# Performance work log

Measured on AMD Instinct MI355X. Metric: run time of the kernel, lower is better.

## Reference

```python
import jax, jax.numpy as jnp
import numpy as np

B, T, F, H = 64, 2048, 256, 256


def setup_inputs() -> dict:
    key = jax.random.key(0)
    k1, k2, k3 = jax.random.split(key, 3)
    return {
        "carry": jnp.zeros((B, H), jnp.float32),
        "x": jax.random.normal(k1, (B, T, F), jnp.float32),
        "Wi": jax.random.normal(k2, (F, 3 * H), jnp.float32) * (1.0 / np.sqrt(F)),
        "Wh": jax.random.normal(k3, (H, 3 * H), jnp.float32) * (1.0 / np.sqrt(H)),
        "bh": jnp.zeros((3 * H,), jnp.float32),
    }


def reference(carry, x, Wi, Wh, bh):
    # time_major=False: transpose to [T, B, F] for the scan
    xt = jnp.transpose(x, (1, 0, 2))
    # Precompute all input projections in one big GEMM (same math as per-step
    # dense_i since inputs don't depend on the carry): [T, B, 3H]
    xi = jnp.einsum("tbf,fg->tbg", xt, Wi)

    def step(h, xi_t):
        hp = h @ Wh + bh  # recurrent projections (bias on hidden side, as in flax GRUCell)
        i_r, i_z, i_n = jnp.split(xi_t, 3, axis=-1)
        h_r, h_z, h_n = jnp.split(hp, 3, axis=-1)
        r = jax.nn.sigmoid(i_r + h_r)
        z = jax.nn.sigmoid(i_z + h_z)
        n = jnp.tanh(i_n + r * h_n)
        new_h = (1.0 - z) * n + z * h
        return new_h, new_h

    carry, hidden = jax.lax.scan(step, carry, xi, unroll=1)
    hidden = jnp.transpose(hidden, (1, 0, 2))  # back to [B, T, H]
    return carry, hidden
```

## Files before the change

kernel.cpp:

```cpp
#include <hip/hip_runtime.h>
#include <hip/hip_fp16.h>
#include <stdint.h>

#define NB   64
#define NT   2048
#define NF   256
#define NH   256
#define NG   768
#define NPROD 192
#define GRPT  16

typedef unsigned int u32;
typedef _Float16 f16;
typedef f16 half2v __attribute__((ext_vector_type(2)));

__device__ __forceinline__ u32 packpair(float a, float b) {
    return __builtin_bit_cast(u32, __builtin_amdgcn_cvt_pkrtz(a, b));
}
__device__ __forceinline__ float fdot2u(u32 w, u32 h, float acc) {
#if __has_builtin(__builtin_amdgcn_fdot2)
    return __builtin_amdgcn_fdot2(__builtin_bit_cast(half2v, w),
                                  __builtin_bit_cast(half2v, h), acc, false);
#else
    half2v wv = __builtin_bit_cast(half2v, w), hv = __builtin_bit_cast(half2v, h);
    return fmaf((float)wv[1], (float)hv[1], fmaf((float)wv[0], (float)hv[0], acc));
#endif
}
__device__ __forceinline__ u32 hfma2u(u32 w, u32 h, u32 acc) {
    __half2 r = __hfma2(__builtin_bit_cast(__half2, w),
                        __builtin_bit_cast(__half2, h),
                        __builtin_bit_cast(__half2, acc));
    return __builtin_bit_cast(u32, r);
}
__device__ __forceinline__ float pairsum(u32 a) {
    __half2 h = __builtin_bit_cast(__half2, a);
    return __low2float(h) + __high2float(h);
}
__device__ __forceinline__ float halfsel(u32 w, int hi) {
    half2v h = __builtin_bit_cast(half2v, w);
    return (float)h[hi & 1];
}
__device__ __forceinline__ float quad_sum(float v) {
    int i = __builtin_bit_cast(int, v);
    v += __builtin_bit_cast(float, __builtin_amdgcn_update_dpp(0, i, 0xB1, 0xF, 0xF, true));
    i = __builtin_bit_cast(int, v);
    v += __builtin_bit_cast(float, __builtin_amdgcn_update_dpp(0, i, 0x4E, 0xF, 0xF, true));
    return v;
}

__global__ __attribute__((amdgpu_flat_work_group_size(1024, 1024),
                          amdgpu_waves_per_eu(4, 4))) void gru_fused(
        const float* __restrict__ carry,
        const float* __restrict__ x,
        const float* __restrict__ Wi,
        const float* __restrict__ Wh,
        const float* __restrict__ bh,
        f16*   __restrict__ xi,
        int*   __restrict__ groups,
        float* __restrict__ out_carry,
        float* __restrict__ out_hidden) {
    const int tid = threadIdx.x;

    if (blockIdx.x >= NB) {
        __shared__ u32 xs2[16][128];
        __shared__ unsigned short ost[16][768];
        const int p = blockIdx.x - NB;

        for (int t = p; t < NT; t += NPROD) {
            #pragma unroll 1
            for (int pass = 0; pass < 4; ++pass) {
                const int b0 = pass * 16;
                for (int i = tid; i < 16 * 128; i += 1024) {
                    const int r = i >> 7, pc = i & 127;
                    const float2 v = *(const float2*)&x[((size_t)(b0 + r) * NT + t) * NF + pc * 2];
                    xs2[r][pc] = packpair(v.x, v.y);
                }
                __syncthreads();

                if (tid < NG) {
                    float acc[16];
                    #pragma unroll
                    for (int r = 0; r < 16; ++r) acc[r] = 0.f;
                    for (int kp = 0; kp < 128; ++kp) {
                        const u32 wp = packpair(Wi[(size_t)(2 * kp) * NG + tid],
                                                Wi[(size_t)(2 * kp + 1) * NG + tid]);
                        #pragma unroll
                        for (int r = 0; r < 16; ++r)
                            acc[r] = fdot2u(wp, xs2[r][kp], acc[r]);
                    }
                    const float bias = (tid < 512) ? bh[tid] : 0.f;
                    #pragma unroll
                    for (int r = 0; r < 16; ++r)
                        ost[r][tid] = (unsigned short)__builtin_bit_cast(unsigned short, (f16)(acc[r] + bias));
                }
                __syncthreads();

                for (int i = tid; i < 16 * 384; i += 1024) {
                    const int r = i / 384, j = i - r * 384;
                    const u32 v = ((const u32*)&ost[r][0])[j];
                    __hip_atomic_store((u32*)xi + ((size_t)(b0 + r) * NT + t) * 384 + j,
                                       v, __ATOMIC_RELAXED, __HIP_MEMORY_SCOPE_AGENT);
                }
                __syncthreads();
            }
            if (tid == 0)
                __hip_atomic_fetch_add(&groups[t >> 4], 1,
                                       __ATOMIC_RELEASE, __HIP_MEMORY_SCOPE_AGENT);
        }
        return;
    }

    __shared__ u32 hsh[2][4][136];
    const int b   = blockIdx.x;
    const int u   = tid >> 2;
    const int kc  = tid & 3;
    const int k0  = kc * 64;

    u32 wh2[3][32];
    #pragma unroll
    for (int j = 0; j < 3; ++j) {
        const float* wp = &Wh[(size_t)k0 * NG + j * 256 + u];
        #pragma unroll
        for (int pp = 0; pp < 32; ++pp) {
            wh2[j][pp] = packpair(wp[0], wp[NG]);
            wp += 2 * (size_t)NG;
        }
    }
    const float bn = bh[512 + u];

    float hreg = carry[(size_t)b * NH + u];
    ((f16*)&hsh[0][kc][0])[u] = (f16)hreg;

    if (tid == 0) {
        while (__hip_atomic_load(&groups[0], __ATOMIC_ACQUIRE, __HIP_MEMORY_SCOPE_AGENT) < GRPT)
            __builtin_amdgcn_s_sleep(2);
    }
    __syncthreads();

    const u32* xb32 = (const u32*)xi + (size_t)b * NT * 384;
    const int  uh   = u >> 1, us = u & 1;
    u32 wr = xb32[uh], wz = xb32[128 + uh], wn = xb32[256 + uh];
    float* op = out_hidden + (size_t)b * NT * NH + u;

#define FMA3(p, hc) { a0 = hfma2u(wh2[0][p], hc, a0); \
                      a1 = hfma2u(wh2[1][p], hc, a1); \
                      a2 = hfma2u(wh2[2][p], hc, a2); }

    for (int t = 0; t < NT; ++t) {
        if (((t + 1) & (GRPT - 1)) == 0 && t + 1 < NT) {
            if (tid == 0) {
                while (__hip_atomic_load(&groups[(t + 1) >> 4], __ATOMIC_ACQUIRE,
                                         __HIP_MEMORY_SCOPE_AGENT) < GRPT)
                    __builtin_amdgcn_s_sleep(2);
            }
            __syncthreads();
        }

        const uint4* hp4 = (const uint4*)&hsh[t & 1][kc][kc * 32];
        u32 a0 = 0, a1 = 0, a2 = 0;
        #pragma unroll
        for (int ph = 0; ph < 4; ++ph) {
            const uint4 hA = hp4[2 * ph], hB = hp4[2 * ph + 1];
            FMA3(8 * ph + 0, hA.x); FMA3(8 * ph + 1, hA.y);
            FMA3(8 * ph + 2, hA.z); FMA3(8 * ph + 3, hA.w);
            FMA3(8 * ph + 4, hB.x); FMA3(8 * ph + 5, hB.y);
            FMA3(8 * ph + 6, hB.z); FMA3(8 * ph + 7, hB.w);
        }
        const float s0 = quad_sum(pairsum(a0));
        const float s1 = quad_sum(pairsum(a1));
        const float s2 = quad_sum(pairsum(a2));

        const float rg = __builtin_amdgcn_rcpf(1.f + __expf(-(halfsel(wr, us) + s0)));
        const float zg = __builtin_amdgcn_rcpf(1.f + __expf(-(halfsel(wz, us) + s1)));
        const float tt = halfsel(wn, us) + rg * (s2 + bn);
        const float ng = 1.f - 2.f * __builtin_amdgcn_rcpf(1.f + __expf(2.f * tt));
        const float hn = ng + zg * (hreg - ng);
        hreg = hn;

        if (kc == 0) *op = hn;
        op += NH;
        ((f16*)&hsh[(t + 1) & 1][kc][0])[u] = (f16)hn;

        if (t + 1 < NT) {
            const size_t base = (size_t)(t + 1) * 384;
            wr = xb32[base + uh]; wz = xb32[base + 128 + uh]; wn = xb32[base + 256 + uh];
        }
        __syncthreads();
    }
#undef FMA3

    if (kc == 0) out_carry[(size_t)b * NH + u] = hreg;
}

extern "C" void kernel_launch(void* const* d_in, const int* in_sizes, int n_in,
                              void* d_out, int out_size, void* d_ws, size_t ws_size,
                              hipStream_t stream) {
    const float* carry = (const float*)d_in[0];
    const float* x     = (const float*)d_in[1];
    const float* Wi    = (const float*)d_in[2];
    const float* Wh    = (const float*)d_in[3];
    const float* bh    = (const float*)d_in[4];

    float* out_carry  = (float*)d_out;
    float* out_hidden = out_carry + (size_t)NB * NH;

    const size_t XI_BYTES = (size_t)NB * NT * NG * 2;
    f16* xi     = (f16*)d_ws;
    int* groups = (int*)((char*)d_ws + XI_BYTES);

    hipMemsetAsync(groups, 0, 128 * sizeof(int), stream);
    gru_fused<<<dim3(NB + NPROD), dim3(1024), 0, stream>>>(
        carry, x, Wi, Wh, bh, xi, groups, out_carry, out_hidden);
}
```

Before: 2.822 ms.

## Store input projections as interleaved fp32 and unroll the recurrent loop per group

The producer blocks now write the input projections to global memory directly as fp32, interleaved as (r,z,n) per hidden unit, instead of staging fp16 values through LDS. Each consumer thread can then fetch its three gate inputs with one vector load. The recurrent dot products switch from packed-half FMA to fdot2 with fp32 accumulation, which drops the pair-sum step and improves accuracy. The time loop is unrolled by the 16-step group so buffer indices are static, and the readiness wait now runs two groups ahead to hide producer latency. In exchange, the xi buffer doubles in size and write traffic, and the last step reads one row past the end of a batch's slice.

```diff
diff --git a/kernel.cpp b/kernel.cpp
--- a/kernel.cpp
+++ b/kernel.cpp
@@ -2,17 +2,19 @@
 #include <hip/hip_fp16.h>
 #include <stdint.h>
 
-#define NB   64
-#define NT   2048
-#define NF   256
-#define NH   256
-#define NG   768
+#define NB    64
+#define NT    2048
+#define NF    256
+#define NH    256
+#define NG    768
 #define NPROD 192
 #define GRPT  16
+#define NGRP  (NT / GRPT)
 
 typedef unsigned int u32;
 typedef _Float16 f16;
 typedef f16 half2v __attribute__((ext_vector_type(2)));
+typedef float f32x4a4 __attribute__((ext_vector_type(4), aligned(4)));
 
 __device__ __forceinline__ u32 packpair(float a, float b) {
     return __builtin_bit_cast(u32, __builtin_amdgcn_cvt_pkrtz(a, b));
@@ -26,20 +28,6 @@
     return fmaf((float)wv[1], (float)hv[1], fmaf((float)wv[0], (float)hv[0], acc));
 #endif
 }
-__device__ __forceinline__ u32 hfma2u(u32 w, u32 h, u32 acc) {
-    __half2 r = __hfma2(__builtin_bit_cast(__half2, w),
-                        __builtin_bit_cast(__half2, h),
-                        __builtin_bit_cast(__half2, acc));
-    return __builtin_bit_cast(u32, r);
-}
-__device__ __forceinline__ float pairsum(u32 a) {
-    __half2 h = __builtin_bit_cast(__half2, a);
-    return __low2float(h) + __high2float(h);
-}
-__device__ __forceinline__ float halfsel(u32 w, int hi) {
-    half2v h = __builtin_bit_cast(half2v, w);
-    return (float)h[hi & 1];
-}
 __device__ __forceinline__ float quad_sum(float v) {
     int i = __builtin_bit_cast(int, v);
     v += __builtin_bit_cast(float, __builtin_amdgcn_update_dpp(0, i, 0xB1, 0xF, 0xF, true));
@@ -55,7 +43,7 @@
         const float* __restrict__ Wi,
         const float* __restrict__ Wh,
         const float* __restrict__ bh,
-        f16*   __restrict__ xi,
+        float* __restrict__ xi,
         int*   __restrict__ groups,
         float* __restrict__ out_carry,
         float* __restrict__ out_hidden) {
@@ -63,7 +51,6 @@
 
     if (blockIdx.x >= NB) {
         __shared__ u32 xs2[16][128];
-        __shared__ unsigned short ost[16][768];
         const int p = blockIdx.x - NB;
 
         for (int t = p; t < NT; t += NPROD) {
@@ -89,17 +76,14 @@
                             acc[r] = fdot2u(wp, xs2[r][kp], acc[r]);
                     }
                     const float bias = (tid < 512) ? bh[tid] : 0.f;
+                    const int g3 = tid >> 8;
+                    const int un = tid & 255;
                     #pragma unroll
-                    for (int r = 0; r < 16; ++r)
-                        ost[r][tid] = (unsigned short)__builtin_bit_cast(unsigned short, (f16)(acc[r] + bias));
-                }
-                __syncthreads();
-
-                for (int i = tid; i < 16 * 384; i += 1024) {
-                    const int r = i / 384, j = i - r * 384;
-                    const u32 v = ((const u32*)&ost[r][0])[j];
-                    __hip_atomic_store((u32*)xi + ((size_t)(b0 + r) * NT + t) * 384 + j,
-                                       v, __ATOMIC_RELAXED, __HIP_MEMORY_SCOPE_AGENT);
+                    for (int r = 0; r < 16; ++r) {
+                        const u32 v = __builtin_bit_cast(u32, acc[r] + bias);
+                        __hip_atomic_store((u32*)xi + ((size_t)(b0 + r) * NT + t) * NG + un * 3 + g3,
+                                           v, __ATOMIC_RELAXED, __HIP_MEMORY_SCOPE_AGENT);
+                    }
                 }
                 __syncthreads();
             }
@@ -134,60 +118,63 @@
     if (tid == 0) {
         while (__hip_atomic_load(&groups[0], __ATOMIC_ACQUIRE, __HIP_MEMORY_SCOPE_AGENT) < GRPT)
             __builtin_amdgcn_s_sleep(2);
+        while (__hip_atomic_load(&groups[1], __ATOMIC_ACQUIRE, __HIP_MEMORY_SCOPE_AGENT) < GRPT)
+            __builtin_amdgcn_s_sleep(2);
     }
     __syncthreads();
 
-    const u32* xb32 = (const u32*)xi + (size_t)b * NT * 384;
-    const int  uh   = u >> 1, us = u & 1;
-    u32 wr = xb32[uh], wz = xb32[128 + uh], wn = xb32[256 + uh];
+    const float* xq = xi + (size_t)b * NT * NG + u * 3;
+    f32x4a4 xv = *(const f32x4a4*)xq;
+    xq += NG;
+    float xr = xv[0], xz = xv[1], xn = xv[2];
     float* op = out_hidden + (size_t)b * NT * NH + u;
 
-#define FMA3(p, hc) { a0 = hfma2u(wh2[0][p], hc, a0); \
-                      a1 = hfma2u(wh2[1][p], hc, a1); \
-                      a2 = hfma2u(wh2[2][p], hc, a2); }
-
-    for (int t = 0; t < NT; ++t) {
-        if (((t + 1) & (GRPT - 1)) == 0 && t + 1 < NT) {
+#define D3(p, hc) { a0 = fdot2u(wh2[0][p], hc, a0); \
+                    a1 = fdot2u(wh2[1][p], hc, a1); \
+                    a2 = fdot2u(wh2[2][p], hc, a2); }
+
+    for (int g = 0; g < NGRP; ++g) {
+        #pragma unroll
+        for (int j = 0; j < GRPT; ++j) {
+            const int RB = j & 1, WB = RB ^ 1;
+            const uint4* hp4 = (const uint4*)&hsh[RB][kc][kc * 32];
+            float a0 = 0.f, a1 = 0.f, a2 = 0.f;
+            #pragma unroll
+            for (int ph = 0; ph < 4; ++ph) {
+                const uint4 hA = hp4[2 * ph], hB = hp4[2 * ph + 1];
+                D3(8 * ph + 0, hA.x); D3(8 * ph + 1, hA.y);
+                D3(8 * ph + 2, hA.z); D3(8 * ph + 3, hA.w);
+                D3(8 * ph + 4, hB.x); D3(8 * ph + 5, hB.y);
+                D3(8 * ph + 6, hB.z); D3(8 * ph + 7, hB.w);
+            }
+            a0 = quad_sum(a0); a1 = quad_sum(a1); a2 = quad_sum(a2);
+
+            const float rg = __builtin_amdgcn_rcpf(1.f + __expf(-(xr + a0)));
+            const float zg = __builtin_amdgcn_rcpf(1.f + __expf(-(xz + a1)));
+            const float tt = xn + rg * (a2 + bn);
+            const float ng = 1.f - 2.f * __builtin_amdgcn_rcpf(1.f + __expf(2.f * tt));
+            const float hn = ng + zg * (hreg - ng);
+            hreg = hn;
+
+            if (kc == 0) *op = hn;
+            op += NH;
+            ((f16*)&hsh[WB][kc][0])[u] = (f16)hn;
+
+            xv = *(const f32x4a4*)xq;
+            xq += NG;
+            xr = xv[0]; xz = xv[1]; xn = xv[2];
+            __syncthreads();
+        }
+        if (g + 2 < NGRP) {
             if (tid == 0) {
-                while (__hip_atomic_load(&groups[(t + 1) >> 4], __ATOMIC_ACQUIRE,
+                while (__hip_atomic_load(&groups[g + 2], __ATOMIC_ACQUIRE,
                                          __HIP_MEMORY_SCOPE_AGENT) < GRPT)
                     __builtin_amdgcn_s_sleep(2);
             }
             __syncthreads();
         }
-
-        const uint4* hp4 = (const uint4*)&hsh[t & 1][kc][kc * 32];
-        u32 a0 = 0, a1 = 0, a2 = 0;
-        #pragma unroll
-        for (int ph = 0; ph < 4; ++ph) {
-            const uint4 hA = hp4[2 * ph], hB = hp4[2 * ph + 1];
-            FMA3(8 * ph + 0, hA.x); FMA3(8 * ph + 1, hA.y);
-            FMA3(8 * ph + 2, hA.z); FMA3(8 * ph + 3, hA.w);
-            FMA3(8 * ph + 4, hB.x); FMA3(8 * ph + 5, hB.y);
-            FMA3(8 * ph + 6, hB.z); FMA3(8 * ph + 7, hB.w);
-        }
-        const float s0 = quad_sum(pairsum(a0));
-        const float s1 = quad_sum(pairsum(a1));
-        const float s2 = quad_sum(pairsum(a2));
-
-        const float rg = __builtin_amdgcn_rcpf(1.f + __expf(-(halfsel(wr, us) + s0)));
-        const float zg = __builtin_amdgcn_rcpf(1.f + __expf(-(halfsel(wz, us) + s1)));
-        const float tt = halfsel(wn, us) + rg * (s2 + bn);
-        const float ng = 1.f - 2.f * __builtin_amdgcn_rcpf(1.f + __expf(2.f * tt));
-        const float hn = ng + zg * (hreg - ng);
-        hreg = hn;
-
-        if (kc == 0) *op = hn;
-        op += NH;
-        ((f16*)&hsh[(t + 1) & 1][kc][0])[u] = (f16)hn;
-
-        if (t + 1 < NT) {
-            const size_t base = (size_t)(t + 1) * 384;
-            wr = xb32[base + uh]; wz = xb32[base + 128 + uh]; wn = xb32[base + 256 + uh];
-        }
-        __syncthreads();
-    }
-#undef FMA3
+    }
+#undef D3
 
     if (kc == 0) out_carry[(size_t)b * NH + u] = hreg;
 }
@@ -204,11 +191,10 @@
     float* out_carry  = (float*)d_out;
     float* out_hidden = out_carry + (size_t)NB * NH;
 
-    const size_t XI_BYTES = (size_t)NB * NT * NG * 2;
-    f16* xi     = (f16*)d_ws;
-    int* groups = (int*)((char*)d_ws + XI_BYTES);
-
-    hipMemsetAsync(groups, 0, 128 * sizeof(int), stream);
+    int*   groups = (int*)d_ws;
+    float* xi     = (float*)((char*)d_ws + 4096);
+
+    hipMemsetAsync(groups, 0, NGRP * sizeof(int), stream);
     gru_fused<<<dim3(NB + NPROD), dim3(1024), 0, stream>>>(
         carry, x, Wi, Wh, bh, xi, groups, out_carry, out_hidden);
 }
```

Measured after the change: 2.518 ms. -10.8%, faster.
